# Kernel tuning notes

Measured on AMD Instinct MI355X. Metric: run time of the kernel, lower is better.

## Reference

```python
import jax, jax.numpy as jnp
import numpy as np

B, N, DIM, H, DH = 2, 1024, 2048, 16, 128
MAX_POS = 16
QK_SCALE = 10.0  # qk_norm_scale (replaces dim_head**-0.5 when qk_norm=True)
NEG = -1e30  # large negative mask value (sigmoid -> 0, softmax -> 0)

def rotate_half(x):
    # interleaved pair rotation: '... (d r) -> ... d r', r=2
    shape = x.shape
    xr = x.reshape(shape[:-1] + (shape[-1] // 2, 2))
    x1, x2 = xr[..., 0], xr[..., 1]
    return jnp.stack((-x2, x1), axis=-1).reshape(shape)

def setup_inputs() -> dict:
    key = jax.random.key(0)
    ks = jax.random.split(key, 10)
    # proper rotary frequencies, repeat-interleaved to match rotate_half's pair layout
    half = DH // 2
    inv_freq = 1.0 / (10000.0 ** (np.arange(half, dtype=np.float32) / half))
    freqs = np.repeat(np.outer(np.arange(N, dtype=np.float32), inv_freq), 2, axis=-1)  # [N, DH]
    sd = 0.02
    return {
        'x': jax.random.normal(ks[0], (B, N, DIM), jnp.float32),
        'rotary_freqs': jnp.asarray(freqs),
        'w_q': jax.random.normal(ks[1], (DIM, H * DH), jnp.float32) * sd,
        'w_k': jax.random.normal(ks[2], (DIM, H * DH), jnp.float32) * sd,
        'w_v': jax.random.normal(ks[3], (DIM, H * DH), jnp.float32) * sd,
        'cope_emb': jax.random.normal(ks[4], (MAX_POS, DH), jnp.float32) * sd,  # CoPE pos_emb (nonzero for testing)
        'th_pre': jnp.eye(H, dtype=jnp.float32) + jax.random.normal(ks[5], (H, H), jnp.float32) * sd,
        'th_post': jnp.eye(H, dtype=jnp.float32) + jax.random.normal(ks[6], (H, H), jnp.float32) * sd,
        'w_vgate': jax.random.normal(ks[7], (DIM, H * DH), jnp.float32) * sd,
        'b_vgate': jnp.full((H * DH,), 10.0, jnp.float32),
        'w_hgate': jax.random.normal(ks[8], (DIM, H), jnp.float32) * sd,
        'b_hgate': jnp.full((H,), 10.0, jnp.float32),
        'w_out': jax.random.normal(ks[9], (H * DH, DIM), jnp.float32) * sd,
    }

def reference(x, rotary_freqs, w_q, w_k, w_v, cope_emb, th_pre, th_post, w_vgate, b_vgate, w_hgate, b_hgate, w_out):
    b, n, _ = x.shape
    to_heads = lambda t: t.reshape(b, n, H, DH).transpose(0, 2, 1, 3)  # b h n d
    q = to_heads(x @ w_q)
    k = to_heads(x @ w_k)
    v = to_heads(x @ w_v)
    # qk l2-norm (groups=1), then fixed qk_norm_scale
    q = q / jnp.maximum(jnp.linalg.norm(q, axis=-1, keepdims=True), 1e-12)
    k = k / jnp.maximum(jnp.linalg.norm(k, axis=-1, keepdims=True), 1e-12)
    # rotary embedding (scale=1, rot_dim == dim_head)
    cos, sin = jnp.cos(rotary_freqs), jnp.sin(rotary_freqs)
    q = q * cos + rotate_half(q) * sin
    k = k * cos + rotate_half(k) * sin
    sim = jnp.einsum('bhid,bhjd->bhij', q, k) * QK_SCALE
    sim = jnp.einsum('hg,bgij->bhij', th_pre, sim)  # pre-softmax talking heads (1x1 conv over heads)
    causal = jnp.triu(jnp.ones((n, n), dtype=bool), 1)
    sim = jnp.where(causal, NEG, sim)
    # ---- CoPE (linear interpolation path) ----
    gates = jax.nn.sigmoid(sim)  # masked entries -> 0
    pos = jnp.flip(jnp.cumsum(jnp.flip(gates, -1), axis=-1), -1)  # reverse cumsum over j
    pos = jnp.minimum(pos, MAX_POS - 1.0)
    logits_int = jnp.einsum('bhnd,pd->bhnp', q, cope_emb)
    pos_floor = jnp.floor(pos)
    w_interp = pos - pos_floor
    lc = jnp.take_along_axis(logits_int, jnp.ceil(pos).astype(jnp.int32), axis=-1)
    lf = jnp.take_along_axis(logits_int, pos_floor.astype(jnp.int32), axis=-1)
    sim = sim + lc * w_interp + lf * (1.0 - w_interp)
    # ------------------------------------------
    attn = jax.nn.softmax(sim, axis=-1)
    attn = jnp.einsum('hg,bgij->bhij', th_post, attn)  # post-softmax talking heads
    out = jnp.einsum('bhij,bhjd->bhid', attn, v)
    # per-head value gate
    head_gate = jax.nn.sigmoid(x @ w_hgate + b_hgate)  # b n h
    out = out * head_gate.transpose(0, 2, 1)[..., None]
    out = out.transpose(0, 2, 1, 3).reshape(b, n, H * DH)
    # elementwise value gate (sigmoid, bias init 10)
    out = out * jax.nn.sigmoid(x @ w_vgate + b_vgate)
    return out @ w_out
```

## Files before the change

kernel.cpp:

```cpp
#include <hip/hip_runtime.h>
#include <hip/hip_fp16.h>

typedef unsigned short u16;
typedef __attribute__((ext_vector_type(4))) float f32x4;
typedef __attribute__((ext_vector_type(8))) _Float16 f16x8;
typedef __attribute__((ext_vector_type(4))) _Float16 f16x4;
typedef __attribute__((ext_vector_type(8))) unsigned short u16x8;
typedef __attribute__((ext_vector_type(4))) unsigned short u16x4;

#define DEVI __device__ __forceinline__
#define MASKV (-1000.0f)

DEVI u16 f2h(float f){ __half h = __float2half(f); return __half_as_ushort(h); }
DEVI float h2f(u16 v){ return __half2float(__ushort_as_half(v)); }
DEVI float sigm(float s){ float e = __expf(-fabsf(s)); return (s >= 0.f) ? 1.f/(1.f+e) : e/(1.f+e); }

DEVI void async16(const void* g, void* l){
  __builtin_amdgcn_global_load_lds((__attribute__((address_space(1))) const unsigned int*)g,
                                   (__attribute__((address_space(3))) unsigned int*)l, 16, 0, 0);
}

struct PrepArgs {
  const float* src[7];
  u16* dst[7];
  int C[7];
};
__global__ __launch_bounds__(256) void k_prep(PrepArgs p){
  __shared__ u16 t[32][33];
  int z = blockIdx.z;
  if (z == 0){
    int i = ((blockIdx.y*64 + blockIdx.x)*256 + threadIdx.x)*4;
    f32x4 v = *(const f32x4*)(p.src[0] + i);
    u16x4 o;
    #pragma unroll
    for (int z2=0; z2<4; z2++) o[z2] = f2h(v[z2]);
    *(u16x4*)(p.dst[0] + i) = o;
    return;
  }
  const float* src = p.src[z]; u16* dst = p.dst[z];
  int R = 2048, C = p.C[z];
  int c0 = blockIdx.x*32, r0 = blockIdx.y*32;
  if (c0 >= C) return;
  int tx = threadIdx.x & 31, ty = threadIdx.x >> 5;
  #pragma unroll
  for (int i = ty; i < 32; i += 8){
    int r = r0 + i, c = c0 + tx;
    if (r < R && c < C) t[i][tx] = f2h(src[(size_t)r*C + c]);
  }
  __syncthreads();
  #pragma unroll
  for (int i = ty; i < 32; i += 8){
    int rr = c0 + i, cc = r0 + tx;
    if (rr < C && cc < R) dst[(size_t)rr*R + cc] = t[tx][i];
  }
}

__global__ __launch_bounds__(256) void k_transpose_h(const u16* __restrict__ src, u16* __restrict__ dst,
    int R, int C, long sps, long dps){
  __shared__ u16 t[32][33];
  src += (size_t)blockIdx.z * sps; dst += (size_t)blockIdx.z * dps;
  int c0 = blockIdx.x*32, r0 = blockIdx.y*32;
  int tx = threadIdx.x & 31, ty = threadIdx.x >> 5;
  #pragma unroll
  for (int i = ty; i < 32; i += 8){
    int r = r0 + i, c = c0 + tx;
    if (r < R && c < C) t[i][tx] = src[(size_t)r*C + c];
  }
  __syncthreads();
  #pragma unroll
  for (int i = ty; i < 32; i += 8){
    int rr = c0 + i, cc = r0 + tx;
    if (rr < C && cc < R) dst[(size_t)rr*R + cc] = t[tx][i];
  }
}

struct ProjArgs {
  const u16* xh;
  const u16* wT0; const u16* wT1; const u16* wT2; const u16* wT3;
  u16* q; u16* k; u16* v; u16* vg;
  const float* bvg;
};
__global__ __launch_bounds__(512) void k_proj2(ProjArgs p){
  __shared__ __align__(16) u16 ldsA[2][16384];
  __shared__ __align__(16) u16 ldsB[2][16384];
  const int z = blockIdx.z;
  const u16* wT = (z==0) ? p.wT0 : (z==1) ? p.wT1 : (z==2) ? p.wT2 : p.wT3;
  const int m0 = blockIdx.x << 8, n0 = blockIdx.y << 8;
  const int tid = threadIdx.x, w = tid >> 6, l = tid & 63;
  const int wm = w >> 2, wn = w & 3, qq = l >> 4, m = l & 15;
  const int cxor = (m & 7) * 8;
  const int lrow = l >> 3;
  const int lcol = (((l & 7) ^ (l >> 3)) * 8);
  const u16* aSrc = p.xh + (size_t)(m0 + lrow) * 2048 + lcol;
  const u16* bSrc = wT   + (size_t)(n0 + lrow) * 2048 + lcol;
  const int wp2 = w * 2;

  f32x4 acc[8][4];
  { f32x4 zr = {0.f,0.f,0.f,0.f};
    #pragma unroll
    for (int i=0;i<8;i++)
      #pragma unroll
      for (int j=0;j<4;j++) acc[i][j] = zr; }

#define STGA(buf,h,kt) do{ \
    async16(aSrc + (size_t)((h)*128 + wp2*8)*2048 + (kt)*64,     &ldsA[buf][(h)*8192 + wp2*512]); \
    async16(aSrc + (size_t)((h)*128 + (wp2+1)*8)*2048 + (kt)*64, &ldsA[buf][(h)*8192 + (wp2+1)*512]); }while(0)
#define STGB(buf,h,kt) do{ \
    async16(bSrc + (size_t)((h)*128 + wp2*8)*2048 + (kt)*64,     &ldsB[buf][(h)*8192 + wp2*512]); \
    async16(bSrc + (size_t)((h)*128 + (wp2+1)*8)*2048 + (kt)*64, &ldsB[buf][(h)*8192 + (wp2+1)*512]); }while(0)
#define RDA(buf,i,s) (*(const f16x8*)(&ldsA[buf][(wm*128 + (i)*16 + m)*64 + (((s)*32 + qq*8) ^ cxor)]))
#define RDB(buf,j,s) (*(const f16x8*)(&ldsB[buf][(wn*64 + (j)*16 + m)*64 + (((s)*32 + qq*8) ^ cxor)]))

  f16x8 bf[4][2];
#define RDBALL(buf) do{ \
    _Pragma("unroll") \
    for (int j=0;j<4;j++){ bf[j][0] = RDB(buf,j,0); bf[j][1] = RDB(buf,j,1); } }while(0)
#define VMW asm volatile("s_waitcnt vmcnt(4)" ::: "memory")
#define PHASE(buf,i0,BSTMT,SSTMT,VMSTMT) do{ \
    f16x8 a00 = RDA(buf,(i0),0),   a01 = RDA(buf,(i0),1); \
    f16x8 a10 = RDA(buf,(i0)+1,0), a11 = RDA(buf,(i0)+1,1); \
    BSTMT; \
    SSTMT; \
    __builtin_amdgcn_s_barrier(); \
    asm volatile("s_waitcnt lgkmcnt(0)" ::: "memory"); \
    __builtin_amdgcn_s_setprio(1); \
    _Pragma("unroll") \
    for (int j=0;j<4;j++){ \
      acc[(i0)][j]   = __builtin_amdgcn_mfma_f32_16x16x32_f16(a00, bf[j][0], acc[(i0)][j],   0,0,0); \
      acc[(i0)][j]   = __builtin_amdgcn_mfma_f32_16x16x32_f16(a01, bf[j][1], acc[(i0)][j],   0,0,0); \
      acc[(i0)+1][j] = __builtin_amdgcn_mfma_f32_16x16x32_f16(a10, bf[j][0], acc[(i0)+1][j], 0,0,0); \
      acc[(i0)+1][j] = __builtin_amdgcn_mfma_f32_16x16x32_f16(a11, bf[j][1], acc[(i0)+1][j], 0,0,0); \
    } \
    __builtin_amdgcn_s_setprio(0); \
    VMSTMT; \
    __builtin_amdgcn_s_barrier(); }while(0)

  STGA(0,0,0); STGA(0,1,0); STGB(0,0,0); STGB(0,1,0); STGB(1,0,1); STGB(1,1,1);
  VMW;
  __builtin_amdgcn_s_barrier();

  for (int u = 0; u < 16; u++){
    const int t1 = 2*u+1, t2 = (2*u+2)&31, t3 = (2*u+3)&31;
    PHASE(0,0, RDBALL(0), STGA(1,0,t1), ((void)0));
    PHASE(0,2, ((void)0), STGA(1,1,t1), ((void)0));
    PHASE(0,4, ((void)0), STGB(0,0,t2), ((void)0));
    PHASE(0,6, ((void)0), STGB(0,1,t2), VMW);
    PHASE(1,0, RDBALL(1), STGA(0,0,t2), ((void)0));
    PHASE(1,2, ((void)0), STGA(0,1,t2), ((void)0));
    PHASE(1,4, ((void)0), STGB(1,0,t3), ((void)0));
    PHASE(1,6, ((void)0), STGB(1,1,t3), VMW);
  }

  u16* dst3 = (z==0) ? p.q : (z==1) ? p.k : p.v;
  #pragma unroll
  for (int i=0;i<8;i++)
  #pragma unroll
  for (int j=0;j<4;j++)
  #pragma unroll
  for (int r=0;r<4;r++){
    int gr = m0 + wm*128 + i*16 + qq*4 + r;
    int gc = n0 + wn*64 + j*16 + m;
    float v = acc[i][j][r];
    if (z == 3){
      p.vg[(size_t)gr*2048 + gc] = f2h(sigm(v + p.bvg[gc]));
    } else {
      int b = gr >> 10, ii = gr & 1023, h = gc >> 7, d = gc & 127;
      dst3[(((size_t)(b*16 + h))*1024 + ii)*128 + d] = f2h(v);
    }
  }
#undef STGA
#undef STGB
#undef RDA
#undef RDB
#undef RDBALL
#undef VMW
#undef PHASE
}

__global__ __launch_bounds__(256) void k_hgate(const u16* __restrict__ xh, const u16* __restrict__ whgT,
    const float* __restrict__ bhg, float* __restrict__ hg){
  __shared__ float red[4][256];
  int tid = threadIdx.x, w = tid>>6, l = tid&63, q = l>>4, m = l&15;
  int t0 = blockIdx.x*16;
  f32x4 acc = {0.f,0.f,0.f,0.f};
  const u16* xr = xh   + (size_t)(t0 + m)*2048 + w*512;
  const u16* br = whgT + (size_t)m*2048 + w*512;
  #pragma unroll 4
  for (int k = 0; k < 512; k += 32){
    f16x8 a = *(const f16x8*)(xr + k + q*8);
    f16x8 b = *(const f16x8*)(br + k + q*8);
    acc = __builtin_amdgcn_mfma_f32_16x16x32_f16(a, b, acc, 0, 0, 0);
  }
  #pragma unroll
  for (int r = 0; r < 4; r++) red[w][(q*4+r)*16 + m] = acc[r];
  __syncthreads();
  float v = red[0][tid] + red[1][tid] + red[2][tid] + red[3][tid];
  int tl = tid >> 4, h = tid & 15;
  hg[(size_t)(t0 + tl)*16 + h] = sigm(v + bhg[h]);
}

__global__ __launch_bounds__(256) void k_normrope(u16* __restrict__ qb, u16* __restrict__ kb,
    const float* __restrict__ freqs, const float* __restrict__ cope, float* __restrict__ L){
  __shared__ float ce[2048];
  int tid = threadIdx.x;
  for (int i2 = tid; i2 < 2048; i2 += 256) ce[i2] = cope[i2];
  __syncthreads();
  int w = tid >> 6, l = tid & 63;
  int r = blockIdx.x*4 + w;
  int isq = (r < 32768) ? 1 : 0;
  int rr = isq ? r : r - 32768;
  int i = rr & 1023;
  u16* base = (isq ? qb : kb) + (size_t)rr*128;
  float v0 = h2f(base[2*l]), v1 = h2f(base[2*l+1]);
  float ss = v0*v0 + v1*v1;
  #pragma unroll
  for (int off = 1; off < 64; off <<= 1) ss += __shfl_xor(ss, off);
  float rn = 1.f / fmaxf(sqrtf(ss), 1e-12f);
  v0 *= rn; v1 *= rn;
  float f = freqs[i*128 + 2*l];
  float sn, cs; sincosf(f, &sn, &cs);
  float o0 = v0*cs - v1*sn, o1 = v1*cs + v0*sn;
  base[2*l] = f2h(o0); base[2*l+1] = f2h(o1);
  if (isq){
    #pragma unroll
    for (int p = 0; p < 16; p++){
      float part = o0*ce[p*128 + 2*l] + o1*ce[p*128 + 2*l + 1];
      #pragma unroll
      for (int off = 1; off < 64; off <<= 1) part += __shfl_xor(part, off);
      if (l == p) L[(size_t)rr*16 + p] = part;
    }
  }
}

__global__ __launch_bounds__(256) void k_qk(const u16* __restrict__ qb, const u16* __restrict__ kb,
    u16* __restrict__ S){
  __shared__ __align__(16) u16 As[8192];
  __shared__ __align__(16) u16 Bs[16384];
  int bh = blockIdx.y;
  int bx = 15 - (int)blockIdx.x;
  int i0 = bx*64, it = bx >> 1;
  int njt = (bx + 2) >> 1;
  int tid = threadIdx.x, w = tid>>6, l = tid&63, q = l>>4, m = l&15, wm = w&1, wn = w>>1;
  const u16* qbase = qb + (size_t)bh*131072;
  const u16* kbase = kb + (size_t)bh*131072;
  #pragma unroll
  for (int sub = 0; sub < 4; sub++){
    int row = w*16 + (l>>2);
    async16(qbase + (size_t)(i0 + row)*128 + sub*32 + (l&3)*8, As + sub*2048 + (w*16)*32);
  }
  u16* dstbase = S + ((size_t)bh*36 + (it*(it+1))/2)*16384 + (size_t)((bx&1)*64)*128;
  for (int jt = 0; jt < njt; jt++){
    __syncthreads();
    #pragma unroll
    for (int sub = 0; sub < 4; sub++)
      #pragma unroll
      for (int p = 0; p < 2; p++){
        int row = w*32 + p*16 + (l>>2);
        async16(kbase + (size_t)(jt*128 + row)*128 + sub*32 + (l&3)*8,
                Bs + sub*4096 + (w*32 + p*16)*32);
      }
    __syncthreads();
    f32x4 acc[2][4];
    { f32x4 z = {0.f,0.f,0.f,0.f};
      #pragma unroll
      for (int a2=0;a2<2;a2++)
        #pragma unroll
        for (int b2=0;b2<4;b2++) acc[a2][b2] = z; }
    #pragma unroll
    for (int kc = 0; kc < 4; kc++){
      f16x8 af[2], bf[4];
      #pragma unroll
      for (int t = 0; t < 2; t++) af[t] = *(const f16x8*)(As + kc*2048 + (wm*32 + t*16 + m)*32 + q*8);
      #pragma unroll
      for (int t = 0; t < 4; t++) bf[t] = *(const f16x8*)(Bs + kc*4096 + (wn*64 + t*16 + m)*32 + q*8);
      #pragma unroll
      for (int a2 = 0; a2 < 2; a2++)
        #pragma unroll
        for (int b2 = 0; b2 < 4; b2++)
          acc[a2][b2] = __builtin_amdgcn_mfma_f32_16x16x32_f16(af[a2], bf[b2], acc[a2][b2], 0, 0, 0);
    }
    u16* dst = dstbase + (size_t)jt*16384;
    #pragma unroll
    for (int ti=0; ti<2; ti++)
    #pragma unroll
    for (int tj=0; tj<4; tj++)
    #pragma unroll
    for (int r=0; r<4; r++){
      int iloc = wm*32 + ti*16 + q*4 + r;
      int jloc = wn*64 + tj*16 + m;
      float v = acc[ti][tj][r] * 10.f;
      if (jt*128 + jloc > i0 + iloc) v = MASKV;
      dst[(size_t)iloc*128 + jloc] = f2h(v);
    }
  }
}

struct CopeArgs { const u16* S; const float* L; const float* thpre; u16* Sout; float* ml; };
__global__ __launch_bounds__(1024) void k_cope(CopeArgs pa){
  __shared__ u16 raw[16*276];
  __shared__ float thsh[256];
  __shared__ float Lsh[1024];
  int b = blockIdx.y;
  int i0 = (int)(gridDim.x - 1 - blockIdx.x) * 4;
  int tid = threadIdx.x, w = tid>>6, l = tid&63;
  int h = w;
  if (tid < 256) thsh[tid] = pa.thpre[tid];
  Lsh[tid] = pa.L[ ((size_t)((b*16 + (tid>>6))*1024) + i0 + ((tid>>4)&3))*16 + (tid&15) ];
  __syncthreads();
  float th_r[16];
  #pragma unroll
  for (int g = 0; g < 16; g++) th_r[g] = thsh[h*16 + g];
  int ii = l >> 4, j0 = (l & 15)*4;
  int i = i0 + ii, it1 = i >> 7, iloc = i & 127;
  const float* Lrow = Lsh + h*64 + ii*16;
  float carry = 0.f, mrun = -1e30f, lrun = 0.f;
  int tmax = (i0 + 3) >> 6;
  for (int t = tmax; t >= 0; t--){
    int jt1 = (t*64) >> 7, jo = (t*64) & 127;
    __syncthreads();
    {
      int e = tid*4;
      int g = e >> 8, r = e & 255;
      int si = r >> 6, j = r & 63;
      int irow = i0 + si; int it2 = irow >> 7, il2 = irow & 127;
      const u16* src = pa.S + ((size_t)((b*16+g)*36 + (it2*(it2+1))/2 + jt1))*16384
                           + (size_t)il2*128 + jo + j;
      *(u16x4*)(raw + g*276 + si*68 + j) = *(const u16x4*)src;
    }
    __syncthreads();
    float s0=0.f, s1=0.f, s2=0.f, s3=0.f;
    #pragma unroll
    for (int g = 0; g < 16; g++){
      u16x4 v = *(const u16x4*)(raw + g*276 + ii*68 + j0);
      float tg = th_r[g];
      s0 += tg*h2f(v[0]); s1 += tg*h2f(v[1]); s2 += tg*h2f(v[2]); s3 += tg*h2f(v[3]);
    }
    float g0 = sigm(s0), g1 = sigm(s1), g2 = sigm(s2), g3 = sigm(s3);
    float c3 = g3, c2 = g2 + c3, c1 = g1 + c2, c0 = g0 + c1;
    float T = c0, Tacc = T;
    #pragma unroll
    for (int off = 1; off < 16; off <<= 1){
      float tv = __shfl(Tacc, (l + off) & 63);
      if (((l & 15) + off) < 16) Tacc += tv;
    }
    float Rh = Tacc - T;
    float rowtot = __shfl(Tacc, l & 48);
    float sf[4];
    float cc[4] = {c0, c1, c2, c3};
    float ssv[4] = {s0, s1, s2, s3};
    #pragma unroll
    for (int c = 0; c < 4; c++){
      float pos = fminf(cc[c] + Rh + carry, 15.f);
      float pf = floorf(pos);
      float wi = pos - pf;
      int ic = (int)ceilf(pos), ifl = (int)pf;
      float v = ssv[c] + Lrow[ic]*wi + Lrow[ifl]*(1.f - wi);
      sf[c] = v;
    }
    carry += rowtot;
    u16x4 ov;
    #pragma unroll
    for (int c = 0; c < 4; c++){ ov[c] = f2h(sf[c]); sf[c] = h2f(ov[c]); }
    *(u16x4*)(pa.Sout + ((size_t)((b*16+h)*36 + (it1*(it1+1))/2 + jt1))*16384
              + (size_t)iloc*128 + jo + j0) = ov;
    float M = fmaxf(fmaxf(sf[0], sf[1]), fmaxf(sf[2], sf[3]));
    #pragma unroll
    for (int off = 1; off < 16; off <<= 1) M = fmaxf(M, __shfl_xor(M, off));
    float mnew = fmaxf(mrun, M);
    float es = __expf(fminf(sf[0]-mnew,0.f)) + __expf(fminf(sf[1]-mnew,0.f))
             + __expf(fminf(sf[2]-mnew,0.f)) + __expf(fminf(sf[3]-mnew,0.f));
    #pragma unroll
    for (int off = 1; off < 16; off <<= 1) es += __shfl_xor(es, off);
    lrun = lrun*__expf(fminf(mrun - mnew, 0.f)) + es;
    mrun = mnew;
  }
  if ((l & 15) == 0){
    size_t bix = (size_t)(b*16 + h)*1024 + i0 + ii;
    pa.ml[bix] = mrun;
    pa.ml[32768 + bix] = 1.f/fmaxf(lrun, 1e-30f);
  }
}

struct PostArgs { const u16* S; const float* ml; const float* thpost; u16* Sout; };
__global__ __launch_bounds__(256) void k_postmix(PostArgs pa){
  __shared__ u16 at[16*1040];
  __shared__ _Float16 thsh[256];
  __shared__ float mh[128], rlh[128];
  int tile = blockIdx.x >> 4, sub = blockIdx.x & 15, b = blockIdx.y;
  int it = 0;
  #pragma unroll
  for (int t2=1; t2<8; t2++) if (tile >= (t2*(t2+1))/2) it = t2;
  int tid = threadIdx.x;
  thsh[tid] = (_Float16)pa.thpost[tid];
  if (tid < 128){
    int g = tid >> 3, ii = tid & 7;
    size_t ix = (size_t)(b*16+g)*1024 + it*128 + sub*8 + ii;
    mh[tid] = pa.ml[ix]; rlh[tid] = pa.ml[32768 + ix];
  }
  __syncthreads();
  {
    int g = tid >> 4, l16 = tid & 15;
    const u16* src = pa.S + ((size_t)((b*16+g)*36 + tile))*16384 + sub*1024;
    #pragma unroll
    for (int c = 0; c < 16; c++){
      int e = c*64 + l16*4;
      int ii = e >> 7;
      float mm = mh[g*8+ii], rr = rlh[g*8+ii];
      u16x4 sv = *(const u16x4*)(src + e);
      u16x4 o;
      #pragma unroll
      for (int z2=0; z2<4; z2++) o[z2] = f2h(__expf(fminf(h2f(sv[z2]) - mm, 0.f)) * rr);
      *(u16x4*)(at + g*1040 + e) = o;
    }
  }
  __syncthreads();
  int h = tid >> 4, c16 = tid & 15;
  _Float16 th_h[16];
  #pragma unroll
  for (int g = 0; g < 16; g++) th_h[g] = thsh[h*16 + g];
  u16* dst = pa.Sout + ((size_t)((b*16+h)*36 + tile))*16384 + sub*1024;
  #pragma unroll
  for (int k = 0; k < 16; k++){
    int e = c16*4 + k*64;
    f16x4 a = {0,0,0,0};
    #pragma unroll
    for (int g = 0; g < 16; g++){
      f16x4 v = *(const f16x4*)(at + g*1040 + e);
      a += v * th_h[g];
    }
    *(f16x4*)(dst + e) = a;
  }
}

struct PvArgs { const u16* S; const u16* vT; const float* hg; const u16* vg; u16* gated; };
__global__ __launch_bounds__(256) void k_pv(PvArgs pa){
  __shared__ __align__(16) u16 As[8192];
  __shared__ __align__(16) u16 Bs[16384];
  int bh = blockIdx.y, b = bh >> 4, h = bh & 15;
  int bx = 15 - (int)blockIdx.x;
  int i0 = bx*64, it = bx >> 1;
  int nc = (bx + 2) >> 1;
  int tid = threadIdx.x, w = tid>>6, l = tid&63, q = l>>4, m = l&15, wm = w&1, wn = w>>1;
  const u16* abase = pa.S + ((size_t)bh*36 + (it*(it+1))/2)*16384 + (size_t)((bx&1)*64)*128;
  const u16* vt    = pa.vT + (size_t)bh*131072;
  f32x4 acc[2][4];
  { f32x4 z = {0.f,0.f,0.f,0.f};
    #pragma unroll
    for (int a2=0;a2<2;a2++)
      #pragma unroll
      for (int b2=0;b2<4;b2++) acc[a2][b2] = z; }
  for (int jc = 0; jc < nc; jc++){
    __syncthreads();
    #pragma unroll
    for (int sub = 0; sub < 4; sub++){
      int row = w*16 + (l>>2);
      async16(abase + (size_t)jc*16384 + (size_t)row*128 + sub*32 + (l&3)*8,
              As + sub*2048 + (w*16)*32);
      #pragma unroll
      for (int p = 0; p < 2; p++){
        int brow = w*32 + p*16 + (l>>2);
        async16(vt + (size_t)brow*1024 + jc*128 + sub*32 + (l&3)*8,
                Bs + sub*4096 + (w*32 + p*16)*32);
      }
    }
    __syncthreads();
    #pragma unroll
    for (int kc = 0; kc < 4; kc++){
      f16x8 af[2], bf[4];
      #pragma unroll
      for (int t = 0; t < 2; t++) af[t] = *(const f16x8*)(As + kc*2048 + (wm*32 + t*16 + m)*32 + q*8);
      #pragma unroll
      for (int t = 0; t < 4; t++) bf[t] = *(const f16x8*)(Bs + kc*4096 + (wn*64 + t*16 + m)*32 + q*8);
      #pragma unroll
      for (int a2 = 0; a2 < 2; a2++)
        #pragma unroll
        for (int b2 = 0; b2 < 4; b2++)
          acc[a2][b2] = __builtin_amdgcn_mfma_f32_16x16x32_f16(af[a2], bf[b2], acc[a2][b2], 0, 0, 0);
    }
  }
  #pragma unroll
  for (int ti=0; ti<2; ti++)
  #pragma unroll
  for (int tj=0; tj<4; tj++)
  #pragma unroll
  for (int r=0; r<4; r++){
    int i = i0 + wm*32 + ti*16 + q*4 + r;
    int d = wn*64 + tj*16 + m;
    int tok = b*1024 + i;
    float v = acc[ti][tj][r] * pa.hg[(size_t)tok*16 + h] * h2f(pa.vg[(size_t)tok*2048 + h*128 + d]);
    if (v != v) v = 333.f;
    pa.gated[(size_t)tok*2048 + h*128 + d] = f2h(v);
  }
}

__global__ __launch_bounds__(256) void k_out(const u16* __restrict__ gated, const u16* __restrict__ woT,
    float* __restrict__ out){
  __shared__ __align__(16) u16 As[2048];
  __shared__ __align__(16) u16 Bs[4096];
  int bx = blockIdx.x;
  int by = blockIdx.y;
  int trow0 = by*64, c0 = bx*128;
  int tid = threadIdx.x, w = tid>>6, l = tid&63, q = l>>4, m = l&15, wm = w&1, wn = w>>1;
  f32x4 acc[2][4];
  { f32x4 z = {0.f,0.f,0.f,0.f};
    #pragma unroll
    for (int a2=0;a2<2;a2++)
      #pragma unroll
      for (int b2=0;b2<4;b2++) acc[a2][b2] = z; }
  for (int k0 = 0; k0 < 2048; k0 += 32){
    __syncthreads();
    {
      int row = w*16 + (l>>2);
      async16(gated + (size_t)(trow0 + row)*2048 + k0 + (l&3)*8, As + (w*16)*32);
    }
    #pragma unroll
    for (int p = 0; p < 2; p++){
      int row = w*32 + p*16 + (l>>2);
      async16(woT + (size_t)(c0 + row)*2048 + k0 + (l&3)*8, Bs + (w*32 + p*16)*32);
    }
    __syncthreads();
    f16x8 af[2], bf[4];
    #pragma unroll
    for (int t = 0; t < 2; t++) af[t] = *(const f16x8*)(As + (wm*32 + t*16 + m)*32 + q*8);
    #pragma unroll
    for (int t = 0; t < 4; t++) bf[t] = *(const f16x8*)(Bs + (wn*64 + t*16 + m)*32 + q*8);
    #pragma unroll
    for (int a2 = 0; a2 < 2; a2++)
      #pragma unroll
      for (int b2 = 0; b2 < 4; b2++)
        acc[a2][b2] = __builtin_amdgcn_mfma_f32_16x16x32_f16(af[a2], bf[b2], acc[a2][b2], 0, 0, 0);
  }
  #pragma unroll
  for (int ti=0; ti<2; ti++)
  #pragma unroll
  for (int tj=0; tj<4; tj++)
  #pragma unroll
  for (int r=0; r<4; r++){
    int trow = trow0 + wm*32 + ti*16 + q*4 + r;
    int col  = c0 + wn*64 + tj*16 + m;
    float o = acc[ti][tj][r];
    if (o != o) o = 911.f;
    out[(size_t)trow*2048 + col] = o;
  }
}

extern "C" void kernel_launch(void* const* d_in, const int* in_sizes, int n_in,
                              void* d_out, int out_size, void* d_ws, size_t ws_size,
                              hipStream_t stream){
  const float* x      = (const float*)d_in[0];
  const float* freqs  = (const float*)d_in[1];
  const float* w_q    = (const float*)d_in[2];
  const float* w_k    = (const float*)d_in[3];
  const float* w_v    = (const float*)d_in[4];
  const float* cope   = (const float*)d_in[5];
  const float* thpre  = (const float*)d_in[6];
  const float* thpost = (const float*)d_in[7];
  const float* w_vg   = (const float*)d_in[8];
  const float* b_vg   = (const float*)d_in[9];
  const float* w_hg   = (const float*)d_in[10];
  const float* b_hg   = (const float*)d_in[11];
  const float* w_out  = (const float*)d_in[12];

  char* ws = (char*)d_ws;
  size_t off = 0;
  auto alloc = [&](size_t bytes)->char*{ char* r = ws + off; off += (bytes + 255) & ~(size_t)255; return r; };
  u16*   xh    = (u16*)  alloc(8388608);
  u16*   wqT   = (u16*)  alloc(8388608);
  u16*   wkT   = (u16*)  alloc(8388608);
  u16*   wvT   = (u16*)  alloc(8388608);
  u16*   wvgT  = (u16*)  alloc(8388608);
  u16*   woT   = (u16*)  alloc(8388608);
  u16*   whgT  = (u16*)  alloc(65536);
  u16*   qb    = (u16*)  alloc(8388608);
  u16*   kb    = (u16*)  alloc(8388608);
  u16*   vb    = (u16*)  alloc(8388608);
  u16*   vTT   = (u16*)  alloc(8388608);
  u16*   vg    = (u16*)  alloc(8388608);
  u16*   gated = (u16*)  alloc(8388608);
  float* L     = (float*)alloc(2097152);
  float* hg    = (float*)alloc(131072);
  float* ml    = (float*)alloc(262144);
  u16*   S     = (u16*)  alloc(37748736);

  dim3 b256(256);
  PrepArgs pp;
  pp.src[0]=x;    pp.dst[0]=xh;   pp.C[0]=2048;
  pp.src[1]=w_q;  pp.dst[1]=wqT;  pp.C[1]=2048;
  pp.src[2]=w_k;  pp.dst[2]=wkT;  pp.C[2]=2048;
  pp.src[3]=w_v;  pp.dst[3]=wvT;  pp.C[3]=2048;
  pp.src[4]=w_vg; pp.dst[4]=wvgT; pp.C[4]=2048;
  pp.src[5]=w_out;pp.dst[5]=woT;  pp.C[5]=2048;
  pp.src[6]=w_hg; pp.dst[6]=whgT; pp.C[6]=16;
  k_prep<<<dim3(64,64,7), b256, 0, stream>>>(pp);

  ProjArgs pa{ xh, wqT, wkT, wvT, wvgT, qb, kb, vb, vg, b_vg };
  k_proj2<<<dim3(8,8,4), dim3(512), 0, stream>>>(pa);
  k_hgate<<<dim3(128), b256, 0, stream>>>(xh, whgT, b_hg, hg);
  k_transpose_h<<<dim3(4,32,32), b256, 0, stream>>>(vb, vTT, 1024, 128, 131072L, 131072L);
  k_normrope<<<dim3(16384), b256, 0, stream>>>(qb, kb, freqs, cope, L);
  k_qk<<<dim3(16,32), b256, 0, stream>>>(qb, kb, S);
  CopeArgs ca{ S, L, thpre, S, ml };
  k_cope<<<dim3(256,2), dim3(1024), 0, stream>>>(ca);
  PostArgs po{ S, ml, thpost, S };
  k_postmix<<<dim3(576,2), b256, 0, stream>>>(po);
  PvArgs pv{ S, vTT, hg, vg, gated };
  k_pv<<<dim3(16,32), b256, 0, stream>>>(pv);
  k_out<<<dim3(16,32), b256, 0, stream>>>(gated, woT, (float*)d_out);
}
```

Baseline: 476.7 us.

## Restructure projection GEMM into triple-buffered K=32 pipeline and widen prep tiles

The fused Q/K/V/vgate projection GEMM drops its double-buffered K=64 phased schedule with XOR-swizzled LDS. It now uses a three-stage ring of K=32 slices: the slice two steps ahead is loaded while the current one is computed, with one barrier per step. Grid axes are also swapped so that blockIdx.x walks the N tiles. The prep kernel moves from 32x32 to 64x64 transpose tiles with float4 loads and 4-wide fp16 stores, and the x-conversion path handles four chunks per block. The unswizzled 64-byte LDS rows may cause bank conflicts, and the smaller K slice adds more barriers relative to the MFMA work.

Result: no change. 480.6 us (+0.8%).

```diff
diff --git a/kernel.cpp b/kernel.cpp
--- a/kernel.cpp
+++ b/kernel.cpp
@@ -26,32 +26,46 @@
   int C[7];
 };
 __global__ __launch_bounds__(256) void k_prep(PrepArgs p){
-  __shared__ u16 t[32][33];
+  __shared__ u16 t[64][65];
   int z = blockIdx.z;
+  int tid = threadIdx.x;
   if (z == 0){
-    int i = ((blockIdx.y*64 + blockIdx.x)*256 + threadIdx.x)*4;
-    f32x4 v = *(const f32x4*)(p.src[0] + i);
-    u16x4 o;
-    #pragma unroll
-    for (int z2=0; z2<4; z2++) o[z2] = f2h(v[z2]);
-    *(u16x4*)(p.dst[0] + i) = o;
+    size_t b0 = (size_t)(blockIdx.y*32 + blockIdx.x)*4096;
+    #pragma unroll
+    for (int c = 0; c < 4; c++){
+      size_t ix = b0 + (size_t)(c*256 + tid)*4;
+      f32x4 v = *(const f32x4*)(p.src[0] + ix);
+      u16x4 o;
+      #pragma unroll
+      for (int e=0; e<4; e++) o[e] = f2h(v[e]);
+      *(u16x4*)(p.dst[0] + ix) = o;
+    }
     return;
   }
   const float* src = p.src[z]; u16* dst = p.dst[z];
-  int R = 2048, C = p.C[z];
-  int c0 = blockIdx.x*32, r0 = blockIdx.y*32;
+  int C = p.C[z];
+  int c0 = blockIdx.x*64, r0 = blockIdx.y*64;
   if (c0 >= C) return;
-  int tx = threadIdx.x & 31, ty = threadIdx.x >> 5;
-  #pragma unroll
-  for (int i = ty; i < 32; i += 8){
-    int r = r0 + i, c = c0 + tx;
-    if (r < R && c < C) t[i][tx] = f2h(src[(size_t)r*C + c]);
+  int tx = tid & 15, ty = tid >> 4;
+  #pragma unroll
+  for (int rr = 0; rr < 4; rr++){
+    int r = r0 + rr*16 + ty, c = c0 + tx*4;
+    if (c < C){
+      f32x4 v = *(const f32x4*)(src + (size_t)r*C + c);
+      #pragma unroll
+      for (int e=0; e<4; e++) t[rr*16+ty][tx*4+e] = f2h(v[e]);
+    }
   }
   __syncthreads();
   #pragma unroll
-  for (int i = ty; i < 32; i += 8){
-    int rr = c0 + i, cc = r0 + tx;
-    if (rr < C && cc < R) dst[(size_t)rr*R + cc] = t[tx][i];
+  for (int rr = 0; rr < 4; rr++){
+    int rr2 = c0 + rr*16 + ty;
+    if (rr2 < C){
+      u16x4 o;
+      #pragma unroll
+      for (int e=0; e<4; e++) o[e] = t[tx*4+e][rr*16+ty];
+      *(u16x4*)(dst + (size_t)rr2*2048 + r0 + tx*4) = o;
+    }
   }
 }
 
@@ -81,19 +95,15 @@
   const float* bvg;
 };
 __global__ __launch_bounds__(512) void k_proj2(ProjArgs p){
-  __shared__ __align__(16) u16 ldsA[2][16384];
-  __shared__ __align__(16) u16 ldsB[2][16384];
+  __shared__ __align__(16) u16 ldsA[3][8192];
+  __shared__ __align__(16) u16 ldsB[3][8192];
   const int z = blockIdx.z;
   const u16* wT = (z==0) ? p.wT0 : (z==1) ? p.wT1 : (z==2) ? p.wT2 : p.wT3;
-  const int m0 = blockIdx.x << 8, n0 = blockIdx.y << 8;
+  const int m0 = blockIdx.y << 8, n0 = blockIdx.x << 8;
   const int tid = threadIdx.x, w = tid >> 6, l = tid & 63;
   const int wm = w >> 2, wn = w & 3, qq = l >> 4, m = l & 15;
-  const int cxor = (m & 7) * 8;
-  const int lrow = l >> 3;
-  const int lcol = (((l & 7) ^ (l >> 3)) * 8);
-  const u16* aSrc = p.xh + (size_t)(m0 + lrow) * 2048 + lcol;
-  const u16* bSrc = wT   + (size_t)(n0 + lrow) * 2048 + lcol;
-  const int wp2 = w * 2;
+  const u16* aS = p.xh + (size_t)(m0 + w*32 + (l>>2)) * 2048 + (l&3)*8;
+  const u16* bS = wT   + (size_t)(n0 + w*32 + (l>>2)) * 2048 + (l&3)*8;
 
   f32x4 acc[8][4];
   { f32x4 zr = {0.f,0.f,0.f,0.f};
@@ -102,54 +112,44 @@
       #pragma unroll
       for (int j=0;j<4;j++) acc[i][j] = zr; }
 
-#define STGA(buf,h,kt) do{ \
-    async16(aSrc + (size_t)((h)*128 + wp2*8)*2048 + (kt)*64,     &ldsA[buf][(h)*8192 + wp2*512]); \
-    async16(aSrc + (size_t)((h)*128 + (wp2+1)*8)*2048 + (kt)*64, &ldsA[buf][(h)*8192 + (wp2+1)*512]); }while(0)
-#define STGB(buf,h,kt) do{ \
-    async16(bSrc + (size_t)((h)*128 + wp2*8)*2048 + (kt)*64,     &ldsB[buf][(h)*8192 + wp2*512]); \
-    async16(bSrc + (size_t)((h)*128 + (wp2+1)*8)*2048 + (kt)*64, &ldsB[buf][(h)*8192 + (wp2+1)*512]); }while(0)
-#define RDA(buf,i,s) (*(const f16x8*)(&ldsA[buf][(wm*128 + (i)*16 + m)*64 + (((s)*32 + qq*8) ^ cxor)]))
-#define RDB(buf,j,s) (*(const f16x8*)(&ldsB[buf][(wn*64 + (j)*16 + m)*64 + (((s)*32 + qq*8) ^ cxor)]))
-
-  f16x8 bf[4][2];
-#define RDBALL(buf) do{ \
+#define STG(buf,kt) do{ \
+    async16(aS + (size_t)(kt)*32,           &ldsA[buf][(w*32)*32]); \
+    async16(aS + (size_t)16*2048 + (size_t)(kt)*32, &ldsA[buf][(w*32+16)*32]); \
+    async16(bS + (size_t)(kt)*32,           &ldsB[buf][(w*32)*32]); \
+    async16(bS + (size_t)16*2048 + (size_t)(kt)*32, &ldsB[buf][(w*32+16)*32]); }while(0)
+
+#define SEGBODY(cur) do{ \
+    f16x8 bf0 = *(const f16x8*)(&ldsB[cur][(wn*64 +  0 + m)*32 + qq*8]); \
+    f16x8 bf1 = *(const f16x8*)(&ldsB[cur][(wn*64 + 16 + m)*32 + qq*8]); \
+    f16x8 bf2 = *(const f16x8*)(&ldsB[cur][(wn*64 + 32 + m)*32 + qq*8]); \
+    f16x8 bf3 = *(const f16x8*)(&ldsB[cur][(wn*64 + 48 + m)*32 + qq*8]); \
     _Pragma("unroll") \
-    for (int j=0;j<4;j++){ bf[j][0] = RDB(buf,j,0); bf[j][1] = RDB(buf,j,1); } }while(0)
-#define VMW asm volatile("s_waitcnt vmcnt(4)" ::: "memory")
-#define PHASE(buf,i0,BSTMT,SSTMT,VMSTMT) do{ \
-    f16x8 a00 = RDA(buf,(i0),0),   a01 = RDA(buf,(i0),1); \
-    f16x8 a10 = RDA(buf,(i0)+1,0), a11 = RDA(buf,(i0)+1,1); \
-    BSTMT; \
-    SSTMT; \
-    __builtin_amdgcn_s_barrier(); \
-    asm volatile("s_waitcnt lgkmcnt(0)" ::: "memory"); \
-    __builtin_amdgcn_s_setprio(1); \
-    _Pragma("unroll") \
-    for (int j=0;j<4;j++){ \
-      acc[(i0)][j]   = __builtin_amdgcn_mfma_f32_16x16x32_f16(a00, bf[j][0], acc[(i0)][j],   0,0,0); \
-      acc[(i0)][j]   = __builtin_amdgcn_mfma_f32_16x16x32_f16(a01, bf[j][1], acc[(i0)][j],   0,0,0); \
-      acc[(i0)+1][j] = __builtin_amdgcn_mfma_f32_16x16x32_f16(a10, bf[j][0], acc[(i0)+1][j], 0,0,0); \
-      acc[(i0)+1][j] = __builtin_amdgcn_mfma_f32_16x16x32_f16(a11, bf[j][1], acc[(i0)+1][j], 0,0,0); \
-    } \
-    __builtin_amdgcn_s_setprio(0); \
-    VMSTMT; \
-    __builtin_amdgcn_s_barrier(); }while(0)
-
-  STGA(0,0,0); STGA(0,1,0); STGB(0,0,0); STGB(0,1,0); STGB(1,0,1); STGB(1,1,1);
-  VMW;
+    for (int i=0;i<8;i++){ \
+      f16x8 a = *(const f16x8*)(&ldsA[cur][(wm*128 + i*16 + m)*32 + qq*8]); \
+      acc[i][0] = __builtin_amdgcn_mfma_f32_16x16x32_f16(a, bf0, acc[i][0], 0,0,0); \
+      acc[i][1] = __builtin_amdgcn_mfma_f32_16x16x32_f16(a, bf1, acc[i][1], 0,0,0); \
+      acc[i][2] = __builtin_amdgcn_mfma_f32_16x16x32_f16(a, bf2, acc[i][2], 0,0,0); \
+      acc[i][3] = __builtin_amdgcn_mfma_f32_16x16x32_f16(a, bf3, acc[i][3], 0,0,0); \
+    } }while(0)
+
+  STG(0,0); STG(1,1);
+  asm volatile("s_waitcnt vmcnt(4)" ::: "memory");
   __builtin_amdgcn_s_barrier();
 
-  for (int u = 0; u < 16; u++){
-    const int t1 = 2*u+1, t2 = (2*u+2)&31, t3 = (2*u+3)&31;
-    PHASE(0,0, RDBALL(0), STGA(1,0,t1), ((void)0));
-    PHASE(0,2, ((void)0), STGA(1,1,t1), ((void)0));
-    PHASE(0,4, ((void)0), STGB(0,0,t2), ((void)0));
-    PHASE(0,6, ((void)0), STGB(0,1,t2), VMW);
-    PHASE(1,0, RDBALL(1), STGA(0,0,t2), ((void)0));
-    PHASE(1,2, ((void)0), STGA(0,1,t2), ((void)0));
-    PHASE(1,4, ((void)0), STGB(1,0,t3), ((void)0));
-    PHASE(1,6, ((void)0), STGB(1,1,t3), VMW);
-  }
+  int cur = 0;
+  for (int t = 0; t < 62; t++){
+    int nb = (cur == 0) ? 2 : cur - 1;
+    STG(nb, t+2);
+    SEGBODY(cur);
+    asm volatile("s_waitcnt vmcnt(4)" ::: "memory");
+    __builtin_amdgcn_s_barrier();
+    cur = (cur == 2) ? 0 : cur + 1;
+  }
+  SEGBODY(cur);
+  asm volatile("s_waitcnt vmcnt(0)" ::: "memory");
+  __builtin_amdgcn_s_barrier();
+  cur = (cur == 2) ? 0 : cur + 1;
+  SEGBODY(cur);
 
   u16* dst3 = (z==0) ? p.q : (z==1) ? p.k : p.v;
   #pragma unroll
@@ -168,13 +168,8 @@
       dst3[(((size_t)(b*16 + h))*1024 + ii)*128 + d] = f2h(v);
     }
   }
-#undef STGA
-#undef STGB
-#undef RDA
-#undef RDB
-#undef RDBALL
-#undef VMW
-#undef PHASE
+#undef STG
+#undef SEGBODY
 }
 
 __global__ __launch_bounds__(256) void k_hgate(const u16* __restrict__ xh, const u16* __restrict__ whgT,
@@ -591,7 +586,7 @@
   pp.src[4]=w_vg; pp.dst[4]=wvgT; pp.C[4]=2048;
   pp.src[5]=w_out;pp.dst[5]=woT;  pp.C[5]=2048;
   pp.src[6]=w_hg; pp.dst[6]=whgT; pp.C[6]=16;
-  k_prep<<<dim3(64,64,7), b256, 0, stream>>>(pp);
+  k_prep<<<dim3(32,32,7), b256, 0, stream>>>(pp);
 
   ProjArgs pa{ xh, wqT, wkT, wvT, wvgT, qb, kb, vb, vg, b_vg };
   k_proj2<<<dim3(8,8,4), dim3(512), 0, stream>>>(pa);
```

## Merge head-gate, V transpose and norm-rope into one launch; widen prep tiles

Applied to the files above, without the earlier changes.

Three independent small kernels (head-gate GEMV, per-head V transpose, q/k l2-norm+rope+CoPE logits) are combined into a single launch that dispatches by block index, removing two kernel launches and their serialization gaps. The weight-prep transpose is changed to 64x64 tiles with float4 loads and 4-wide half stores, and the x cast processes 4 vectors per thread. The projection GEMM grid swaps its x/y mapping of M and N tiles, changing block scheduling order. The merged kernel carries the union of shared memory (about 13KB), which could lower occupancy for the lightweight paths.

Result: faster. 455.0 us (-4.6%).

```diff
diff --git a/kernel.cpp b/kernel.cpp
--- a/kernel.cpp
+++ b/kernel.cpp
@@ -26,51 +26,46 @@
   int C[7];
 };
 __global__ __launch_bounds__(256) void k_prep(PrepArgs p){
-  __shared__ u16 t[32][33];
+  __shared__ u16 t[64][65];
   int z = blockIdx.z;
+  int tid = threadIdx.x;
   if (z == 0){
-    int i = ((blockIdx.y*64 + blockIdx.x)*256 + threadIdx.x)*4;
-    f32x4 v = *(const f32x4*)(p.src[0] + i);
-    u16x4 o;
-    #pragma unroll
-    for (int z2=0; z2<4; z2++) o[z2] = f2h(v[z2]);
-    *(u16x4*)(p.dst[0] + i) = o;
+    size_t b0 = (size_t)(blockIdx.y*32 + blockIdx.x)*4096;
+    #pragma unroll
+    for (int c = 0; c < 4; c++){
+      size_t ix = b0 + (size_t)(c*256 + tid)*4;
+      f32x4 v = *(const f32x4*)(p.src[0] + ix);
+      u16x4 o;
+      #pragma unroll
+      for (int e=0; e<4; e++) o[e] = f2h(v[e]);
+      *(u16x4*)(p.dst[0] + ix) = o;
+    }
     return;
   }
   const float* src = p.src[z]; u16* dst = p.dst[z];
-  int R = 2048, C = p.C[z];
-  int c0 = blockIdx.x*32, r0 = blockIdx.y*32;
+  int C = p.C[z];
+  int c0 = blockIdx.x*64, r0 = blockIdx.y*64;
   if (c0 >= C) return;
-  int tx = threadIdx.x & 31, ty = threadIdx.x >> 5;
-  #pragma unroll
-  for (int i = ty; i < 32; i += 8){
-    int r = r0 + i, c = c0 + tx;
-    if (r < R && c < C) t[i][tx] = f2h(src[(size_t)r*C + c]);
+  int tx = tid & 15, ty = tid >> 4;
+  #pragma unroll
+  for (int rr = 0; rr < 4; rr++){
+    int r = r0 + rr*16 + ty, c = c0 + tx*4;
+    if (c < C){
+      f32x4 v = *(const f32x4*)(src + (size_t)r*C + c);
+      #pragma unroll
+      for (int e=0; e<4; e++) t[rr*16+ty][tx*4+e] = f2h(v[e]);
+    }
   }
   __syncthreads();
   #pragma unroll
-  for (int i = ty; i < 32; i += 8){
-    int rr = c0 + i, cc = r0 + tx;
-    if (rr < C && cc < R) dst[(size_t)rr*R + cc] = t[tx][i];
-  }
-}
-
-__global__ __launch_bounds__(256) void k_transpose_h(const u16* __restrict__ src, u16* __restrict__ dst,
-    int R, int C, long sps, long dps){
-  __shared__ u16 t[32][33];
-  src += (size_t)blockIdx.z * sps; dst += (size_t)blockIdx.z * dps;
-  int c0 = blockIdx.x*32, r0 = blockIdx.y*32;
-  int tx = threadIdx.x & 31, ty = threadIdx.x >> 5;
-  #pragma unroll
-  for (int i = ty; i < 32; i += 8){
-    int r = r0 + i, c = c0 + tx;
-    if (r < R && c < C) t[i][tx] = src[(size_t)r*C + c];
-  }
-  __syncthreads();
-  #pragma unroll
-  for (int i = ty; i < 32; i += 8){
-    int rr = c0 + i, cc = r0 + tx;
-    if (rr < C && cc < R) dst[(size_t)rr*R + cc] = t[tx][i];
+  for (int rr = 0; rr < 4; rr++){
+    int rr2 = c0 + rr*16 + ty;
+    if (rr2 < C){
+      u16x4 o;
+      #pragma unroll
+      for (int e=0; e<4; e++) o[e] = t[tx*4+e][rr*16+ty];
+      *(u16x4*)(dst + (size_t)rr2*2048 + r0 + tx*4) = o;
+    }
   }
 }
 
@@ -85,7 +80,7 @@
   __shared__ __align__(16) u16 ldsB[2][16384];
   const int z = blockIdx.z;
   const u16* wT = (z==0) ? p.wT0 : (z==1) ? p.wT1 : (z==2) ? p.wT2 : p.wT3;
-  const int m0 = blockIdx.x << 8, n0 = blockIdx.y << 8;
+  const int m0 = blockIdx.y << 8, n0 = blockIdx.x << 8;
   const int tid = threadIdx.x, w = tid >> 6, l = tid & 63;
   const int wm = w >> 2, wn = w & 3, qq = l >> 4, m = l & 15;
   const int cxor = (m & 7) * 8;
@@ -177,57 +172,86 @@
 #undef PHASE
 }
 
-__global__ __launch_bounds__(256) void k_hgate(const u16* __restrict__ xh, const u16* __restrict__ whgT,
-    const float* __restrict__ bhg, float* __restrict__ hg){
+struct MidArgs {
+  const u16* xh; const u16* whgT; const float* bhg; float* hg;
+  const u16* vb; u16* vTT;
+  u16* qb; u16* kb; const float* freqs; const float* cope; float* L;
+};
+__global__ __launch_bounds__(256) void k_mid(MidArgs p){
   __shared__ float red[4][256];
-  int tid = threadIdx.x, w = tid>>6, l = tid&63, q = l>>4, m = l&15;
-  int t0 = blockIdx.x*16;
-  f32x4 acc = {0.f,0.f,0.f,0.f};
-  const u16* xr = xh   + (size_t)(t0 + m)*2048 + w*512;
-  const u16* br = whgT + (size_t)m*2048 + w*512;
-  #pragma unroll 4
-  for (int k = 0; k < 512; k += 32){
-    f16x8 a = *(const f16x8*)(xr + k + q*8);
-    f16x8 b = *(const f16x8*)(br + k + q*8);
-    acc = __builtin_amdgcn_mfma_f32_16x16x32_f16(a, b, acc, 0, 0, 0);
-  }
-  #pragma unroll
-  for (int r = 0; r < 4; r++) red[w][(q*4+r)*16 + m] = acc[r];
-  __syncthreads();
-  float v = red[0][tid] + red[1][tid] + red[2][tid] + red[3][tid];
-  int tl = tid >> 4, h = tid & 15;
-  hg[(size_t)(t0 + tl)*16 + h] = sigm(v + bhg[h]);
-}
-
-__global__ __launch_bounds__(256) void k_normrope(u16* __restrict__ qb, u16* __restrict__ kb,
-    const float* __restrict__ freqs, const float* __restrict__ cope, float* __restrict__ L){
+  __shared__ u16 t[32][33];
   __shared__ float ce[2048];
+  int bz = blockIdx.x;
   int tid = threadIdx.x;
-  for (int i2 = tid; i2 < 2048; i2 += 256) ce[i2] = cope[i2];
-  __syncthreads();
-  int w = tid >> 6, l = tid & 63;
-  int r = blockIdx.x*4 + w;
-  int isq = (r < 32768) ? 1 : 0;
-  int rr = isq ? r : r - 32768;
-  int i = rr & 1023;
-  u16* base = (isq ? qb : kb) + (size_t)rr*128;
-  float v0 = h2f(base[2*l]), v1 = h2f(base[2*l+1]);
-  float ss = v0*v0 + v1*v1;
-  #pragma unroll
-  for (int off = 1; off < 64; off <<= 1) ss += __shfl_xor(ss, off);
-  float rn = 1.f / fmaxf(sqrtf(ss), 1e-12f);
-  v0 *= rn; v1 *= rn;
-  float f = freqs[i*128 + 2*l];
-  float sn, cs; sincosf(f, &sn, &cs);
-  float o0 = v0*cs - v1*sn, o1 = v1*cs + v0*sn;
-  base[2*l] = f2h(o0); base[2*l+1] = f2h(o1);
-  if (isq){
-    #pragma unroll
-    for (int p = 0; p < 16; p++){
-      float part = o0*ce[p*128 + 2*l] + o1*ce[p*128 + 2*l + 1];
-      #pragma unroll
-      for (int off = 1; off < 64; off <<= 1) part += __shfl_xor(part, off);
-      if (l == p) L[(size_t)rr*16 + p] = part;
+  if (bz < 128){
+    int w = tid>>6, l = tid&63, q = l>>4, m = l&15;
+    int t0 = bz*16;
+    f32x4 acc = {0.f,0.f,0.f,0.f};
+    const u16* xr = p.xh   + (size_t)(t0 + m)*2048 + w*512;
+    const u16* br = p.whgT + (size_t)m*2048 + w*512;
+    #pragma unroll 4
+    for (int k = 0; k < 512; k += 32){
+      f16x8 a = *(const f16x8*)(xr + k + q*8);
+      f16x8 b = *(const f16x8*)(br + k + q*8);
+      acc = __builtin_amdgcn_mfma_f32_16x16x32_f16(a, b, acc, 0, 0, 0);
+    }
+    #pragma unroll
+    for (int r = 0; r < 4; r++) red[w][(q*4+r)*16 + m] = acc[r];
+    __syncthreads();
+    float v = red[0][tid] + red[1][tid] + red[2][tid] + red[3][tid];
+    int tl = tid >> 4, h = tid & 15;
+    p.hg[(size_t)(t0 + tl)*16 + h] = sigm(v + p.bhg[h]);
+    return;
+  }
+  if (bz < 4224){
+    int f = bz - 128;
+    int zb = f >> 7, rem = f & 127;
+    int by = rem >> 2, bx = rem & 3;
+    const u16* src = p.vb + (size_t)zb*131072;
+    u16* dst = p.vTT + (size_t)zb*131072;
+    int c0 = bx*32, r0 = by*32;
+    int tx = tid & 31, ty = tid >> 5;
+    #pragma unroll
+    for (int i = ty; i < 32; i += 8){
+      int r = r0 + i, c = c0 + tx;
+      t[i][tx] = src[(size_t)r*128 + c];
+    }
+    __syncthreads();
+    #pragma unroll
+    for (int i = ty; i < 32; i += 8){
+      int rr = c0 + i, cc = r0 + tx;
+      dst[(size_t)rr*1024 + cc] = t[tx][i];
+    }
+    return;
+  }
+  {
+    int bx = bz - 4224;
+    for (int i2 = tid; i2 < 2048; i2 += 256) ce[i2] = p.cope[i2];
+    __syncthreads();
+    int w = tid >> 6, l = tid & 63;
+    int r = bx*4 + w;
+    int isq = (r < 32768) ? 1 : 0;
+    int rr = isq ? r : r - 32768;
+    int i = rr & 1023;
+    u16* base = (isq ? p.qb : p.kb) + (size_t)rr*128;
+    float v0 = h2f(base[2*l]), v1 = h2f(base[2*l+1]);
+    float ss = v0*v0 + v1*v1;
+    #pragma unroll
+    for (int off = 1; off < 64; off <<= 1) ss += __shfl_xor(ss, off);
+    float rn = 1.f / fmaxf(sqrtf(ss), 1e-12f);
+    v0 *= rn; v1 *= rn;
+    float f = p.freqs[i*128 + 2*l];
+    float sn, cs; sincosf(f, &sn, &cs);
+    float o0 = v0*cs - v1*sn, o1 = v1*cs + v0*sn;
+    base[2*l] = f2h(o0); base[2*l+1] = f2h(o1);
+    if (isq){
+      #pragma unroll
+      for (int pp = 0; pp < 16; pp++){
+        float part = o0*ce[pp*128 + 2*l] + o1*ce[pp*128 + 2*l + 1];
+        #pragma unroll
+        for (int off = 1; off < 64; off <<= 1) part += __shfl_xor(part, off);
+        if (l == pp) p.L[(size_t)rr*16 + pp] = part;
+      }
     }
   }
 }
@@ -591,13 +615,12 @@
   pp.src[4]=w_vg; pp.dst[4]=wvgT; pp.C[4]=2048;
   pp.src[5]=w_out;pp.dst[5]=woT;  pp.C[5]=2048;
   pp.src[6]=w_hg; pp.dst[6]=whgT; pp.C[6]=16;
-  k_prep<<<dim3(64,64,7), b256, 0, stream>>>(pp);
+  k_prep<<<dim3(32,32,7), b256, 0, stream>>>(pp);
 
   ProjArgs pa{ xh, wqT, wkT, wvT, wvgT, qb, kb, vb, vg, b_vg };
   k_proj2<<<dim3(8,8,4), dim3(512), 0, stream>>>(pa);
-  k_hgate<<<dim3(128), b256, 0, stream>>>(xh, whgT, b_hg, hg);
-  k_transpose_h<<<dim3(4,32,32), b256, 0, stream>>>(vb, vTT, 1024, 128, 131072L, 131072L);
-  k_normrope<<<dim3(16384), b256, 0, stream>>>(qb, kb, freqs, cope, L);
+  MidArgs ma{ xh, whgT, b_hg, hg, vb, vTT, qb, kb, freqs, cope, L };
+  k_mid<<<dim3(20608), b256, 0, stream>>>(ma);
   k_qk<<<dim3(16,32), b256, 0, stream>>>(qb, kb, S);
   CopeArgs ca{ S, L, thpre, S, ml };
   k_cope<<<dim3(256,2), dim3(1024), 0, stream>>>(ca);
```
